# Optimization experiments

Hardware: AMD Instinct MI355X
Metric: run time of the kernel (lower is better)

## Reference

```python
import jax, jax.numpy as jnp
import numpy as np

BS, D, H = 65536, 768, 12
DK = D // H // 2  # 32
EPS = 1e-6

def setup_inputs() -> dict:
    key = jax.random.key(0)
    ks = jax.random.split(key, 4)
    scale = 1.0 / np.sqrt(D)
    return {
        "x": jax.random.normal(ks[0], (BS, D), dtype=jnp.float32),
        "Wq": jax.random.normal(ks[1], (D, D), dtype=jnp.float32) * scale,
        "Wk": jax.random.normal(ks[2], (D, D), dtype=jnp.float32) * scale,
        "Wv": jax.random.normal(ks[3], (D, D), dtype=jnp.float32) * scale,
        "gamma": jnp.ones((D,), dtype=jnp.float32),
        "beta": jnp.zeros((D,), dtype=jnp.float32),
    }

def reference(x, Wq, Wk, Wv, gamma, beta):
    bs = x.shape[0]
    # LayerNorm (eps=1e-6)
    mu = jnp.mean(x, axis=-1, keepdims=True)
    var = jnp.mean(jnp.square(x - mu), axis=-1, keepdims=True)
    xn = (x - mu) / jnp.sqrt(var + EPS) * gamma + beta
    # QKV projections (nn.Linear, no bias: y = x @ W.T), split feature dim as (h, 2, d_k)
    q = (xn @ Wq.T).reshape(bs, H, 2, DK)
    k = (xn @ Wk.T).reshape(bs, H, 2, DK)
    v = (xn @ Wv.T).reshape(bs, H, 2, DK)
    # tiny 2x2 attention per head
    scores = jnp.einsum('bhpd,bhqd->bhpq', q, k) / np.sqrt(DK)
    attn = jax.nn.softmax(scores, axis=-1)
    out = jnp.einsum('bhpq,bhqd->bhpd', attn, v).reshape(bs, D)
    return out + x
```

## Files before the change

kernel.cpp:

```cpp
#include <hip/hip_runtime.h>

typedef _Float16 f16;
typedef _Float16 f16x8 __attribute__((ext_vector_type(8)));
typedef _Float16 f16x4 __attribute__((ext_vector_type(4)));
typedef float f32x16 __attribute__((ext_vector_type(16)));

#define BS 65536
#define D 768
#define H 12
#define RB 128
#define NBLK ((BS / RB) * H)
#define W_ELEMS ((size_t)D * D)
#define XN_ELEMS ((size_t)BS * D)

typedef const __attribute__((address_space(1))) void gvoid_t;
typedef __attribute__((address_space(3))) void lvoid_t;

__global__ __launch_bounds__(256, 4) void ln_kernel(const float* __restrict__ x,
                                                    const float* __restrict__ gamma,
                                                    const float* __restrict__ beta,
                                                    f16* __restrict__ xn) {
  __shared__ f16 sRow[4][2 * D];
  int wave = threadIdx.x >> 6, lane = threadIdx.x & 63;
  size_t row0 = ((size_t)blockIdx.x * 4 + wave) * 2;
  const float4* xr0 = (const float4*)(x + row0 * D) + lane * 3;
  const float4* xr1 = (const float4*)(x + (row0 + 1) * D) + lane * 3;
  float4 u0 = xr0[0], u1 = xr0[1], u2 = xr0[2];
  float4 w0 = xr1[0], w1 = xr1[1], w2 = xr1[2];

  float s0 = (u0.x + u0.y) + (u0.z + u0.w) + (u1.x + u1.y) + (u1.z + u1.w)
           + (u2.x + u2.y) + (u2.z + u2.w);
  float q0 = u0.x*u0.x + u0.y*u0.y + u0.z*u0.z + u0.w*u0.w
           + u1.x*u1.x + u1.y*u1.y + u1.z*u1.z + u1.w*u1.w
           + u2.x*u2.x + u2.y*u2.y + u2.z*u2.z + u2.w*u2.w;
  float s1 = (w0.x + w0.y) + (w0.z + w0.w) + (w1.x + w1.y) + (w1.z + w1.w)
           + (w2.x + w2.y) + (w2.z + w2.w);
  float q1 = w0.x*w0.x + w0.y*w0.y + w0.z*w0.z + w0.w*w0.w
           + w1.x*w1.x + w1.y*w1.y + w1.z*w1.z + w1.w*w1.w
           + w2.x*w2.x + w2.y*w2.y + w2.z*w2.z + w2.w*w2.w;
#pragma unroll
  for (int d2 = 1; d2 <= 32; d2 <<= 1) {
    s0 += __shfl_xor(s0, d2, 64); q0 += __shfl_xor(q0, d2, 64);
    s1 += __shfl_xor(s1, d2, 64); q1 += __shfl_xor(q1, d2, 64);
  }
  float mu0 = s0 * (1.0f / D), rs0 = rsqrtf(q0 * (1.0f / D) - mu0 * mu0 + 1e-6f);
  float mu1 = s1 * (1.0f / D), rs1 = rsqrtf(q1 * (1.0f / D) - mu1 * mu1 + 1e-6f);

  const float4* g4 = (const float4*)(gamma) + lane * 3;
  const float4* b4 = (const float4*)(beta)  + lane * 3;
  float4 g0 = g4[0], g1 = g4[1], g2 = g4[2];
  float4 b0 = b4[0], b1 = b4[1], b2 = b4[2];

  f16* sw = &sRow[wave][lane * 12];
#define NRM4(dst, off, V, G, B, MU, RS)                        \
  { f16x4 o;                                                   \
    o[0] = (f16)((V.x - MU) * RS * G.x + B.x);                 \
    o[1] = (f16)((V.y - MU) * RS * G.y + B.y);                 \
    o[2] = (f16)((V.z - MU) * RS * G.z + B.z);                 \
    o[3] = (f16)((V.w - MU) * RS * G.w + B.w);                 \
    *(f16x4*)(dst + off) = o; }
  NRM4(sw, 0, u0, g0, b0, mu0, rs0)
  NRM4(sw, 4, u1, g1, b1, mu0, rs0)
  NRM4(sw, 8, u2, g2, b2, mu0, rs0)
  NRM4(sw, D + 0, w0, g0, b0, mu1, rs1)
  NRM4(sw, D + 4, w1, g1, b1, mu1, rs1)
  NRM4(sw, D + 8, w2, g2, b2, mu1, rs1)
#undef NRM4
  __builtin_amdgcn_sched_barrier(0);
  asm volatile("s_waitcnt lgkmcnt(0)" ::: "memory");
  __builtin_amdgcn_sched_barrier(0);
  f16* xo = xn + row0 * D;
#pragma unroll
  for (int j = 0; j < 3; ++j) {
    int c = j * 64 + lane;
    f16x8 v = *(const f16x8*)(&sRow[wave][c * 8]);
    *(f16x8*)(xo + c * 8) = v;
  }
}

__global__ __launch_bounds__(256, 4) void wconv_kernel(const float* __restrict__ Wq,
                                                       const float* __restrict__ Wk,
                                                       const float* __restrict__ Wv,
                                                       f16* __restrict__ wf) {
  int b = blockIdx.x;
  int m = b / 288;
  size_t e = ((size_t)(b % 288) * 256 + threadIdx.x) * 8;
  const float* src = (m == 0 ? Wq : (m == 1 ? Wk : Wv)) + e;
  float4 v0 = *(const float4*)src;
  float4 v1 = *(const float4*)(src + 4);
  f16x8 o;
  o[0] = (f16)v0.x; o[1] = (f16)v0.y; o[2] = (f16)v0.z; o[3] = (f16)v0.w;
  o[4] = (f16)v1.x; o[5] = (f16)v1.y; o[6] = (f16)v1.z; o[7] = (f16)v1.w;
  *(f16x8*)(wf + (size_t)m * W_ELEMS + e) = o;
}

__global__ __launch_bounds__(256, 2) void qkv_attn_kernel(const f16* __restrict__ xn,
                                                          const f16* __restrict__ wf,
                                                          const float* __restrict__ x,
                                                          float* __restrict__ out) {
  __shared__ f16 sA[2][RB * 64]  __attribute__((aligned(16)));
  __shared__ f16 sB[2][192 * 64] __attribute__((aligned(16)));

  const int tid  = threadIdx.x;
  const int wave = tid >> 6;
  const int lane = tid & 63;
  const int l31  = lane & 31;
  const int hi   = lane >> 5;

  int bid = blockIdx.x;
  int my  = (bid & 7) * (NBLK / 8) + (bid >> 3);
  int rb  = my / H;
  int h   = my % H;

  const int ri = lane >> 3;
  const int ci = lane & 7;

  const f16* abase = xn + (size_t)rb * RB * D;
  unsigned aoffs[4];
#pragma unroll
  for (int o = 0; o < 4; ++o)
    aoffs[o] = (unsigned)((wave * 32 + o * 8 + ri) * D + ((ci ^ ri) * 8));

  unsigned boffs[6];
#pragma unroll
  for (int o = 0; o < 6; ++o) {
    int n = wave * 48 + o * 8 + ri;
    boffs[o] = (unsigned)((n >> 6) * (int)W_ELEMS + (h * 64 + (n & 63)) * D + ((ci ^ ri) * 8));
  }

  const int q7 = l31 & 7;
  int aoff[4], coff[4];
#pragma unroll
  for (int s = 0; s < 4; ++s) {
    int kc = s * 2 + hi;
    aoff[s] = (wave * 32 + l31) * 64 + ((kc ^ q7) * 8);
    coff[s] = l31 * 64 + ((kc ^ q7) * 8);
  }

#define STAGE(KO, BUF)                                                                   \
  {                                                                                      \
    _Pragma("unroll") for (int o = 0; o < 4; ++o) {                                      \
      __builtin_amdgcn_global_load_lds((gvoid_t*)(abase + aoffs[o] + (KO) * 64),         \
                                       (lvoid_t*)(&sA[BUF][(wave * 32 + o * 8) * 64]),   \
                                       16, 0, 0);                                        \
    }                                                                                    \
    _Pragma("unroll") for (int o = 0; o < 6; ++o) {                                      \
      __builtin_amdgcn_global_load_lds((gvoid_t*)(wf + boffs[o] + (KO) * 64),            \
                                       (lvoid_t*)(&sB[BUF][(wave * 48 + o * 8) * 64]),   \
                                       16, 0, 0);                                        \
    }                                                                                    \
  }

  STAGE(0, 0);

  f32x16 acc[6];
#pragma unroll
  for (int t = 0; t < 6; ++t)
#pragma unroll
    for (int i = 0; i < 16; ++i) acc[t][i] = 0.f;

#pragma unroll
  for (int ko = 0; ko < 12; ++ko) {
    const int cur = ko & 1;
    if (ko < 11) STAGE(ko + 1, cur ^ 1);

    if (ko < 11) asm volatile("s_waitcnt vmcnt(10)\n\ts_barrier" ::: "memory");
    else         asm volatile("s_waitcnt vmcnt(0)\n\ts_barrier" ::: "memory");

    __builtin_amdgcn_s_setprio(1);
#pragma unroll
    for (int s = 0; s < 4; ++s) {
      f16x8 a = *(const f16x8*)(&sA[cur][aoff[s]]);
#pragma unroll
      for (int t = 0; t < 6; ++t) {
        f16x8 b = *(const f16x8*)(&sB[cur][coff[s] + t * 2048]);
        acc[t] = __builtin_amdgcn_mfma_f32_32x32x16_f16(a, b, acc[t], 0, 0, 0);
      }
    }
    __builtin_amdgcn_s_setprio(0);

    if (ko < 11) asm volatile("s_barrier" ::: "memory");
  }

  {
    const size_t grow0 = (size_t)rb * RB + wave * 32;
    const float scale = 0.17677669529663687f;
#pragma unroll
    for (int g = 0; g < 16; ++g) {
      float q0 = acc[0][g], q1 = acc[1][g];
      float k0 = acc[2][g], k1 = acc[3][g];
      float s00 = q0 * k0, s01 = q0 * k1, s10 = q1 * k0, s11 = q1 * k1;
#pragma unroll
      for (int d2 = 1; d2 <= 16; d2 <<= 1) {
        s00 += __shfl_xor(s00, d2, 64);
        s01 += __shfl_xor(s01, d2, 64);
        s10 += __shfl_xor(s10, d2, 64);
        s11 += __shfl_xor(s11, d2, 64);
      }
      s00 *= scale; s01 *= scale; s10 *= scale; s11 *= scale;
      float mx0 = fmaxf(s00, s01);
      float e00 = __expf(s00 - mx0), e01 = __expf(s01 - mx0);
      float r0 = 1.0f / (e00 + e01);
      float a00 = e00 * r0, a01 = e01 * r0;
      float mx1 = fmaxf(s10, s11);
      float e10 = __expf(s10 - mx1), e11 = __expf(s11 - mx1);
      float r1 = 1.0f / (e10 + e11);
      float a10 = e10 * r1, a11 = e11 * r1;

      int row_w = (g & 3) + 8 * (g >> 2) + 4 * hi;
      const float* xp = x   + (grow0 + row_w) * D + h * 64 + l31;
      float*       op = out + (grow0 + row_w) * D + h * 64 + l31;
      float v0 = acc[4][g], v1 = acc[5][g];
      op[0]  = a00 * v0 + a01 * v1 + xp[0];
      op[32] = a10 * v0 + a11 * v1 + xp[32];
    }
  }
#undef STAGE
}

extern "C" void kernel_launch(void* const* d_in, const int* in_sizes, int n_in,
                              void* d_out, int out_size, void* d_ws, size_t ws_size,
                              hipStream_t stream) {
  const float* x     = (const float*)d_in[0];
  const float* Wq    = (const float*)d_in[1];
  const float* Wk    = (const float*)d_in[2];
  const float* Wv    = (const float*)d_in[3];
  const float* gamma = (const float*)d_in[4];
  const float* beta  = (const float*)d_in[5];
  float* out = (float*)d_out;
  (void)in_sizes; (void)n_in; (void)out_size; (void)ws_size;

  f16* xn = (f16*)d_ws;
  f16* wf = xn + XN_ELEMS;

  ln_kernel<<<dim3(BS / 8), dim3(256), 0, stream>>>(x, gamma, beta, xn);
  wconv_kernel<<<dim3(864), dim3(256), 0, stream>>>(Wq, Wk, Wv, wf);
  qkv_attn_kernel<<<dim3(NBLK), dim3(256), 0, stream>>>(xn, wf, x, out);
}
```

Measured before the change: 723.4 us.

## Pre-swizzle normalized activations into MFMA fragment layout and load A operand directly

The LayerNorm kernel now writes xn in a packed layout matching the MFMA A-fragment order. The GEMM kernel can then load A fragments straight from global memory into registers instead of staging them through LDS. This removes the sA buffer and its LDS traffic and shrinks shared memory, so launch bounds rise to 3 blocks per CU. The trade-offs are per-lane global loads in the main loop, adjusted waitcnt and barrier logic, and a LayerNorm kernel that strides rows across threads with less coalesced reads.

Result: faster. 643.8 us (-11.0%).

```diff
diff --git a/kernel.cpp b/kernel.cpp
--- a/kernel.cpp
+++ b/kernel.cpp
@@ -2,7 +2,6 @@
 
 typedef _Float16 f16;
 typedef _Float16 f16x8 __attribute__((ext_vector_type(8)));
-typedef _Float16 f16x4 __attribute__((ext_vector_type(4)));
 typedef float f32x16 __attribute__((ext_vector_type(16)));
 
 #define BS 65536
@@ -16,65 +15,55 @@
 typedef const __attribute__((address_space(1))) void gvoid_t;
 typedef __attribute__((address_space(3))) void lvoid_t;
 
+
 __global__ __launch_bounds__(256, 4) void ln_kernel(const float* __restrict__ x,
                                                     const float* __restrict__ gamma,
                                                     const float* __restrict__ beta,
-                                                    f16* __restrict__ xn) {
-  __shared__ f16 sRow[4][2 * D];
-  int wave = threadIdx.x >> 6, lane = threadIdx.x & 63;
-  size_t row0 = ((size_t)blockIdx.x * 4 + wave) * 2;
-  const float4* xr0 = (const float4*)(x + row0 * D) + lane * 3;
-  const float4* xr1 = (const float4*)(x + (row0 + 1) * D) + lane * 3;
-  float4 u0 = xr0[0], u1 = xr0[1], u2 = xr0[2];
-  float4 w0 = xr1[0], w1 = xr1[1], w2 = xr1[2];
-
-  float s0 = (u0.x + u0.y) + (u0.z + u0.w) + (u1.x + u1.y) + (u1.z + u1.w)
-           + (u2.x + u2.y) + (u2.z + u2.w);
-  float q0 = u0.x*u0.x + u0.y*u0.y + u0.z*u0.z + u0.w*u0.w
-           + u1.x*u1.x + u1.y*u1.y + u1.z*u1.z + u1.w*u1.w
-           + u2.x*u2.x + u2.y*u2.y + u2.z*u2.z + u2.w*u2.w;
-  float s1 = (w0.x + w0.y) + (w0.z + w0.w) + (w1.x + w1.y) + (w1.z + w1.w)
-           + (w2.x + w2.y) + (w2.z + w2.w);
-  float q1 = w0.x*w0.x + w0.y*w0.y + w0.z*w0.z + w0.w*w0.w
-           + w1.x*w1.x + w1.y*w1.y + w1.z*w1.z + w1.w*w1.w
-           + w2.x*w2.x + w2.y*w2.y + w2.z*w2.z + w2.w*w2.w;
-#pragma unroll
-  for (int d2 = 1; d2 <= 32; d2 <<= 1) {
-    s0 += __shfl_xor(s0, d2, 64); q0 += __shfl_xor(q0, d2, 64);
-    s1 += __shfl_xor(s1, d2, 64); q1 += __shfl_xor(q1, d2, 64);
-  }
-  float mu0 = s0 * (1.0f / D), rs0 = rsqrtf(q0 * (1.0f / D) - mu0 * mu0 + 1e-6f);
-  float mu1 = s1 * (1.0f / D), rs1 = rsqrtf(q1 * (1.0f / D) - mu1 * mu1 + 1e-6f);
-
-  const float4* g4 = (const float4*)(gamma) + lane * 3;
-  const float4* b4 = (const float4*)(beta)  + lane * 3;
-  float4 g0 = g4[0], g1 = g4[1], g2 = g4[2];
-  float4 b0 = b4[0], b1 = b4[1], b2 = b4[2];
-
-  f16* sw = &sRow[wave][lane * 12];
-#define NRM4(dst, off, V, G, B, MU, RS)                        \
-  { f16x4 o;                                                   \
-    o[0] = (f16)((V.x - MU) * RS * G.x + B.x);                 \
-    o[1] = (f16)((V.y - MU) * RS * G.y + B.y);                 \
-    o[2] = (f16)((V.z - MU) * RS * G.z + B.z);                 \
-    o[3] = (f16)((V.w - MU) * RS * G.w + B.w);                 \
-    *(f16x4*)(dst + off) = o; }
-  NRM4(sw, 0, u0, g0, b0, mu0, rs0)
-  NRM4(sw, 4, u1, g1, b1, mu0, rs0)
-  NRM4(sw, 8, u2, g2, b2, mu0, rs0)
-  NRM4(sw, D + 0, w0, g0, b0, mu1, rs1)
-  NRM4(sw, D + 4, w1, g1, b1, mu1, rs1)
-  NRM4(sw, D + 8, w2, g2, b2, mu1, rs1)
-#undef NRM4
-  __builtin_amdgcn_sched_barrier(0);
-  asm volatile("s_waitcnt lgkmcnt(0)" ::: "memory");
-  __builtin_amdgcn_sched_barrier(0);
-  f16* xo = xn + row0 * D;
-#pragma unroll
-  for (int j = 0; j < 3; ++j) {
-    int c = j * 64 + lane;
-    f16x8 v = *(const f16x8*)(&sRow[wave][c * 8]);
-    *(f16x8*)(xo + c * 8) = v;
+                                                    f16* __restrict__ xp) {
+  __shared__ float sSum[16][17], sSq[16][17];
+  const int tid = threadIdx.x;
+  const int r  = tid & 15;
+  const int sg = tid >> 4;
+  const size_t R = (size_t)blockIdx.x * 16 + r;
+  const float4* xs = (const float4*)(x + R * D + sg * 48);
+  float4 v[12];
+  float sum = 0.f, sq = 0.f;
+#pragma unroll
+  for (int j = 0; j < 12; ++j) {
+    v[j] = xs[j];
+    sum += (v[j].x + v[j].y) + (v[j].z + v[j].w);
+    sq  += v[j].x * v[j].x + v[j].y * v[j].y + v[j].z * v[j].z + v[j].w * v[j].w;
+  }
+  sSum[sg][r] = sum; sSq[sg][r] = sq;
+  __syncthreads();
+  float ts = 0.f, tq = 0.f;
+#pragma unroll
+  for (int k = 0; k < 16; ++k) { ts += sSum[k][r]; tq += sSq[k][r]; }
+  const float mu   = ts * (1.0f / D);
+  const float rstd = rsqrtf(tq * (1.0f / D) - mu * mu + 1e-6f);
+
+  const float4* g4 = (const float4*)(gamma + sg * 48);
+  const float4* b4 = (const float4*)(beta  + sg * 48);
+  const int rb12 = (int)(R >> 5) * 12;
+  const int r31  = (int)(R & 31);
+#pragma unroll
+  for (int jj = 0; jj < 6; ++jj) {
+    const int k = sg * 48 + jj * 8;
+    float4 g0 = g4[2 * jj], g1 = g4[2 * jj + 1];
+    float4 b0 = b4[2 * jj], b1 = b4[2 * jj + 1];
+    float4 u0 = v[2 * jj],  u1 = v[2 * jj + 1];
+    f16x8 o;
+    o[0] = (f16)((u0.x - mu) * rstd * g0.x + b0.x);
+    o[1] = (f16)((u0.y - mu) * rstd * g0.y + b0.y);
+    o[2] = (f16)((u0.z - mu) * rstd * g0.z + b0.z);
+    o[3] = (f16)((u0.w - mu) * rstd * g0.w + b0.w);
+    o[4] = (f16)((u1.x - mu) * rstd * g1.x + b1.x);
+    o[5] = (f16)((u1.y - mu) * rstd * g1.y + b1.y);
+    o[6] = (f16)((u1.z - mu) * rstd * g1.z + b1.z);
+    o[7] = (f16)((u1.w - mu) * rstd * g1.w + b1.w);
+    size_t addr = ((size_t)(rb12 + (k >> 6))) * 2048 + ((k >> 4) & 3) * 512
+                + ((k >> 3) & 1) * 256 + r31 * 8;
+    *(f16x8*)(xp + addr) = o;
   }
 }
 
@@ -94,11 +83,10 @@
   *(f16x8*)(wf + (size_t)m * W_ELEMS + e) = o;
 }
 
-__global__ __launch_bounds__(256, 2) void qkv_attn_kernel(const f16* __restrict__ xn,
+__global__ __launch_bounds__(256, 3) void qkv_attn_kernel(const f16* __restrict__ xp,
                                                           const f16* __restrict__ wf,
                                                           const float* __restrict__ x,
                                                           float* __restrict__ out) {
-  __shared__ f16 sA[2][RB * 64]  __attribute__((aligned(16)));
   __shared__ f16 sB[2][192 * 64] __attribute__((aligned(16)));
 
   const int tid  = threadIdx.x;
@@ -115,12 +103,6 @@
   const int ri = lane >> 3;
   const int ci = lane & 7;
 
-  const f16* abase = xn + (size_t)rb * RB * D;
-  unsigned aoffs[4];
-#pragma unroll
-  for (int o = 0; o < 4; ++o)
-    aoffs[o] = (unsigned)((wave * 32 + o * 8 + ri) * D + ((ci ^ ri) * 8));
-
   unsigned boffs[6];
 #pragma unroll
   for (int o = 0; o < 6; ++o) {
@@ -129,21 +111,14 @@
   }
 
   const int q7 = l31 & 7;
-  int aoff[4], coff[4];
-#pragma unroll
-  for (int s = 0; s < 4; ++s) {
-    int kc = s * 2 + hi;
-    aoff[s] = (wave * 32 + l31) * 64 + ((kc ^ q7) * 8);
-    coff[s] = l31 * 64 + ((kc ^ q7) * 8);
-  }
+  int coff[4];
+#pragma unroll
+  for (int s = 0; s < 4; ++s) coff[s] = l31 * 64 + (((s * 2 + hi) ^ q7) * 8);
+
+  const f16* ap = xp + ((size_t)(rb * 4 + wave) * 12) * 2048 + hi * 256 + l31 * 8;
 
 #define STAGE(KO, BUF)                                                                   \
   {                                                                                      \
-    _Pragma("unroll") for (int o = 0; o < 4; ++o) {                                      \
-      __builtin_amdgcn_global_load_lds((gvoid_t*)(abase + aoffs[o] + (KO) * 64),         \
-                                       (lvoid_t*)(&sA[BUF][(wave * 32 + o * 8) * 64]),   \
-                                       16, 0, 0);                                        \
-    }                                                                                    \
     _Pragma("unroll") for (int o = 0; o < 6; ++o) {                                      \
       __builtin_amdgcn_global_load_lds((gvoid_t*)(wf + boffs[o] + (KO) * 64),            \
                                        (lvoid_t*)(&sB[BUF][(wave * 48 + o * 8) * 64]),   \
@@ -162,24 +137,50 @@
 #pragma unroll
   for (int ko = 0; ko < 12; ++ko) {
     const int cur = ko & 1;
+
+    f16x8 a0 = *(const f16x8*)(ap + ko * 2048);
+    f16x8 a1 = *(const f16x8*)(ap + ko * 2048 + 512);
+    f16x8 a2 = *(const f16x8*)(ap + ko * 2048 + 1024);
+    f16x8 a3 = *(const f16x8*)(ap + ko * 2048 + 1536);
+    __builtin_amdgcn_sched_barrier(0);
     if (ko < 11) STAGE(ko + 1, cur ^ 1);
-
-    if (ko < 11) asm volatile("s_waitcnt vmcnt(10)\n\ts_barrier" ::: "memory");
-    else         asm volatile("s_waitcnt vmcnt(0)\n\ts_barrier" ::: "memory");
+    __builtin_amdgcn_sched_barrier(0);
+    if (ko < 11) asm volatile("s_waitcnt vmcnt(10)" ::: "memory");
+    else         asm volatile("s_waitcnt vmcnt(4)" ::: "memory");
+    __builtin_amdgcn_sched_barrier(0);
+    __builtin_amdgcn_s_barrier();
 
     __builtin_amdgcn_s_setprio(1);
-#pragma unroll
-    for (int s = 0; s < 4; ++s) {
-      f16x8 a = *(const f16x8*)(&sA[cur][aoff[s]]);
-#pragma unroll
-      for (int t = 0; t < 6; ++t) {
-        f16x8 b = *(const f16x8*)(&sB[cur][coff[s] + t * 2048]);
-        acc[t] = __builtin_amdgcn_mfma_f32_32x32x16_f16(a, b, acc[t], 0, 0, 0);
+    {
+      f16x8 b;
+#pragma unroll
+      for (int t = 0; t < 6; ++t) {
+        b = *(const f16x8*)(&sB[cur][coff[0] + t * 2048]);
+        acc[t] = __builtin_amdgcn_mfma_f32_32x32x16_f16(a0, b, acc[t], 0, 0, 0);
+      }
+#pragma unroll
+      for (int t = 0; t < 6; ++t) {
+        b = *(const f16x8*)(&sB[cur][coff[1] + t * 2048]);
+        acc[t] = __builtin_amdgcn_mfma_f32_32x32x16_f16(a1, b, acc[t], 0, 0, 0);
+      }
+#pragma unroll
+      for (int t = 0; t < 6; ++t) {
+        b = *(const f16x8*)(&sB[cur][coff[2] + t * 2048]);
+        acc[t] = __builtin_amdgcn_mfma_f32_32x32x16_f16(a2, b, acc[t], 0, 0, 0);
+      }
+#pragma unroll
+      for (int t = 0; t < 6; ++t) {
+        b = *(const f16x8*)(&sB[cur][coff[3] + t * 2048]);
+        acc[t] = __builtin_amdgcn_mfma_f32_32x32x16_f16(a3, b, acc[t], 0, 0, 0);
       }
     }
     __builtin_amdgcn_s_setprio(0);
 
-    if (ko < 11) asm volatile("s_barrier" ::: "memory");
+    if (ko < 11) {
+      asm volatile("s_waitcnt lgkmcnt(0)" ::: "memory");
+      __builtin_amdgcn_sched_barrier(0);
+      __builtin_amdgcn_s_barrier();
+    }
   }
 
   {
@@ -208,11 +209,11 @@
       float a10 = e10 * r1, a11 = e11 * r1;
 
       int row_w = (g & 3) + 8 * (g >> 2) + 4 * hi;
-      const float* xp = x   + (grow0 + row_w) * D + h * 64 + l31;
+      const float* xq = x   + (grow0 + row_w) * D + h * 64 + l31;
       float*       op = out + (grow0 + row_w) * D + h * 64 + l31;
       float v0 = acc[4][g], v1 = acc[5][g];
-      op[0]  = a00 * v0 + a01 * v1 + xp[0];
-      op[32] = a10 * v0 + a11 * v1 + xp[32];
+      op[0]  = a00 * v0 + a01 * v1 + xq[0];
+      op[32] = a10 * v0 + a11 * v1 + xq[32];
     }
   }
 #undef STAGE
@@ -230,10 +231,10 @@
   float* out = (float*)d_out;
   (void)in_sizes; (void)n_in; (void)out_size; (void)ws_size;
 
-  f16* xn = (f16*)d_ws;
-  f16* wf = xn + XN_ELEMS;
-
-  ln_kernel<<<dim3(BS / 8), dim3(256), 0, stream>>>(x, gamma, beta, xn);
+  f16* xp = (f16*)d_ws;
+  f16* wf = xp + XN_ELEMS;
+
+  ln_kernel<<<dim3(BS / 16), dim3(256), 0, stream>>>(x, gamma, beta, xp);
   wconv_kernel<<<dim3(864), dim3(256), 0, stream>>>(Wq, Wk, Wv, wf);
-  qkv_attn_kernel<<<dim3(NBLK), dim3(256), 0, stream>>>(xn, wf, x, out);
-}
+  qkv_attn_kernel<<<dim3(NBLK), dim3(256), 0, stream>>>(xp, wf, x, out);
+}
```
